# Kernel tuning notes

Measured on AMD Instinct MI355X. Metric: run time of the kernel, lower is better.

## Reference

```python
import jax, jax.numpy as jnp
import numpy as np
from jax import lax

N_TRACES = 128
TRACE_LEN = 32          # uniform trace length -> seq_len
INPUT_DIM = 64
HIDDEN_DIM = 128
BATCH = N_TRACES * TRACE_LEN  # 4096 events = batch_size


def setup_inputs() -> dict:
    key = jax.random.key(0)
    ks = jax.random.split(key, 12)
    s = 1.0 / np.sqrt(HIDDEN_DIM)
    u = lambda k, shape: jax.random.uniform(k, shape, jnp.float32, -s, s)
    return {
        "input": jax.random.normal(ks[0], (BATCH, INPUT_DIM), jnp.float32),
        # layer 0 LSTM params (gate order i,f,g,o as in torch)
        "W_ih0": u(ks[1], (4 * HIDDEN_DIM, INPUT_DIM)),
        "W_hh0": u(ks[2], (4 * HIDDEN_DIM, HIDDEN_DIM)),
        "b_ih0": u(ks[3], (4 * HIDDEN_DIM,)),
        "b_hh0": u(ks[4], (4 * HIDDEN_DIM,)),
        # layer 1 LSTM params
        "W_ih1": u(ks[5], (4 * HIDDEN_DIM, HIDDEN_DIM)),
        "W_hh1": u(ks[6], (4 * HIDDEN_DIM, HIDDEN_DIM)),
        "b_ih1": u(ks[7], (4 * HIDDEN_DIM,)),
        "b_hh1": u(ks[8], (4 * HIDDEN_DIM,)),
        # final linear: hidden -> 1
        "W_lin": u(ks[9], (1, HIDDEN_DIM)),
        "b_lin": u(ks[10], (1,)),
    }


def _lstm_layer(xs, W_ih, W_hh, b_ih, b_hh):
    # xs: [T, B, D_in] time-major. Returns hidden stream [T, B, H].
    H = W_hh.shape[1]
    B = xs.shape[1]
    # precompute input projection for all timesteps
    x_proj = jnp.einsum('tbd,gd->tbg', xs, W_ih) + b_ih + b_hh  # [T,B,4H]

    def step(carry, xp):
        h, c = carry
        gates = xp + h @ W_hh.T                # [B,4H]
        i, f, g, o = jnp.split(gates, 4, axis=-1)
        i = jax.nn.sigmoid(i)
        f = jax.nn.sigmoid(f)
        g = jnp.tanh(g)
        o = jax.nn.sigmoid(o)
        c = f * c + i * g
        h = o * jnp.tanh(c)
        return (h, c), h

    h0 = jnp.zeros((B, H), xs.dtype)
    _, hs = lax.scan(step, (h0, h0), x_proj)
    return hs


def _forward(input, W_ih0, W_hh0, b_ih0, b_hh0, W_ih1, W_hh1, b_ih1, b_hh1, W_lin, b_lin):
    L, D = TRACE_LEN, INPUT_DIM
    # Prefix scatter: event k of a trace gets the padded prefix events[0..k].
    x_tr = input.reshape(N_TRACES, L, D)                       # [Ntr, L, D]
    causal = (jnp.arange(L)[None, :] <= jnp.arange(L)[:, None])  # [k, j] mask j<=k
    padded = x_tr[:, None, :, :] * causal[None, :, :, None].astype(input.dtype)  # [Ntr,L(k),L(j),D]
    padded = padded.reshape(BATCH, L, D)                       # batch-first padded sequences

    xs = jnp.transpose(padded, (1, 0, 2))                      # [L, B, D] time-major
    h1 = _lstm_layer(xs, W_ih0, W_hh0, b_ih0, b_hh0)           # [L, B, H]
    h2 = _lstm_layer(h1, W_ih1, W_hh1, b_ih1, b_hh1)           # [L, B, H]

    out = jnp.einsum('tbh,oh->tbo', h2, W_lin) + b_lin         # [L, B, 1]
    # last valid timestep gather: lengths[i]-1 = (i mod L)
    lens_m1 = jnp.tile(jnp.arange(L), N_TRACES)                # [B]
    y_pred = out[lens_m1, jnp.arange(BATCH), 0]                # [B]
    return y_pred


def reference(input, W_ih0, W_hh0, b_ih0, b_hh0, W_ih1, W_hh1, b_ih1, b_hh1, W_lin, b_lin):
    return _forward(input, W_ih0, W_hh0, b_ih0, b_hh0, W_ih1, W_hh1, b_ih1, b_hh1, W_lin, b_lin)
```

## Files before the change

kernel.cpp:

```cpp
#include <hip/hip_runtime.h>

#define N_TRACES 128
#define TLEN 32
#define IN_DIM 64
#define HID 128
#define G4 (4 * HID)
#define BATCH (N_TRACES * TLEN)
#define HROW 160


__device__ __forceinline__ float fast_sigmoid(float x) {
    return 1.0f / (1.0f + __expf(-x));
}
__device__ __forceinline__ float fast_tanh(float x) {
    return 1.0f - 2.0f / (__expf(2.0f * x) + 1.0f);
}
__device__ __forceinline__ float oct_reduce(float x) {
    x += __int_as_float(__builtin_amdgcn_update_dpp(
        0, __float_as_int(x), 0xB1 , 0xF, 0xF, true));
    x += __int_as_float(__builtin_amdgcn_update_dpp(
        0, __float_as_int(x), 0x4E , 0xF, 0xF, true));
    x += __int_as_float(__builtin_amdgcn_update_dpp(
        0, __float_as_int(x), 0x141 , 0xF, 0xF, true));
    return x;
}

__device__ __forceinline__ void load_w16(const float* __restrict__ W, int u, int s,
                                         float (&w)[4][16]) {
    #pragma unroll
    for (int i = 0; i < 4; ++i) {
        const float* wr = W + (size_t)(u + 128 * i) * HID + 16 * s;
        #pragma unroll
        for (int j = 0; j < 4; ++j) {
            float4 v = *(const float4*)(wr + 4 * j);
            w[i][4 * j + 0] = v.x; w[i][4 * j + 1] = v.y;
            w[i][4 * j + 2] = v.z; w[i][4 * j + 3] = v.w;
        }
    }
    #pragma unroll
    for (int i = 0; i < 4; ++i)
        #pragma unroll
        for (int j = 0; j < 16; ++j)
            asm volatile("" : "+v"(w[i][j]));
}

__device__ __forceinline__ void matvec_acc16(const float (&w)[4][16],
                                             const float* hb, float (&acc)[4]) {
    #pragma unroll
    for (int j = 0; j < 4; ++j) {
        float4 v = *(const float4*)(hb + 4 * j);
        float hx[4] = {v.x, v.y, v.z, v.w};
        #pragma unroll
        for (int e = 0; e < 4; ++e) {
            #pragma unroll
            for (int i = 0; i < 4; ++i)
                acc[i] = fmaf(w[i][4 * j + e], hx[e], acc[i]);
        }
    }
}


template <int K>
__global__ __launch_bounds__(256) void gemm_bt(
    const float* __restrict__ A,
    const float* __restrict__ W,
    const float* __restrict__ b1,
    const float* __restrict__ b2,
    float* __restrict__ out,
    int Nld)
{
    constexpr int LD = 68;
    __shared__ float At[K][LD];
    __shared__ float Wt[K][LD];

    const int tid = threadIdx.x;
    const int m0 = blockIdx.x * 64;
    const int n0 = blockIdx.y * 64;

    const int rot = tid & 3;
    #pragma unroll
    for (int j = 0; j < K / 16; ++j) {
        const int e = 4 * (tid + 256 * j);
        const int row = e / K;
        const int k = e % K;
        float4 va = *(const float4*)(A + (size_t)(m0 + row) * K + k);
        float4 vw = *(const float4*)(W + (size_t)(n0 + row) * K + k);
        float fa[4] = {va.x, va.y, va.z, va.w};
        float fw[4] = {vw.x, vw.y, vw.z, vw.w};
        #pragma unroll
        for (int ii = 0; ii < 4; ++ii) {
            const int i = (ii + rot) & 3;
            At[k + i][row] = fa[i];
            Wt[k + i][row] = fw[i];
        }
    }
    __syncthreads();

    const int tx = tid & 15;
    const int ty = tid >> 4;
    float acc[4][4] = {};

    #pragma unroll 4
    for (int k = 0; k < K; ++k) {
        float4 a = *(const float4*)&At[k][ty * 4];
        float4 w = *(const float4*)&Wt[k][tx * 4];
        acc[0][0] = fmaf(a.x, w.x, acc[0][0]); acc[0][1] = fmaf(a.x, w.y, acc[0][1]);
        acc[0][2] = fmaf(a.x, w.z, acc[0][2]); acc[0][3] = fmaf(a.x, w.w, acc[0][3]);
        acc[1][0] = fmaf(a.y, w.x, acc[1][0]); acc[1][1] = fmaf(a.y, w.y, acc[1][1]);
        acc[1][2] = fmaf(a.y, w.z, acc[1][2]); acc[1][3] = fmaf(a.y, w.w, acc[1][3]);
        acc[2][0] = fmaf(a.z, w.x, acc[2][0]); acc[2][1] = fmaf(a.z, w.y, acc[2][1]);
        acc[2][2] = fmaf(a.z, w.z, acc[2][2]); acc[2][3] = fmaf(a.z, w.w, acc[2][3]);
        acc[3][0] = fmaf(a.w, w.x, acc[3][0]); acc[3][1] = fmaf(a.w, w.y, acc[3][1]);
        acc[3][2] = fmaf(a.w, w.z, acc[3][2]); acc[3][3] = fmaf(a.w, w.w, acc[3][3]);
    }

    float bb[4];
    #pragma unroll
    for (int j = 0; j < 4; ++j) {
        const int n = n0 + tx * 4 + j;
        bb[j] = b1[n] + b2[n];
    }
    #pragma unroll
    for (int i = 0; i < 4; ++i) {
        const int m = m0 + ty * 4 + i;
        float4 v;
        v.x = acc[i][0] + bb[0]; v.y = acc[i][1] + bb[1];
        v.z = acc[i][2] + bb[2]; v.w = acc[i][3] + bb[3];
        *(float4*)(out + (size_t)m * Nld + n0 + tx * 4) = v;
    }
}


__global__ __launch_bounds__(1024) void fused_trace(
    const float* __restrict__ xproj0,
    const float* __restrict__ Whh0,
    const float* __restrict__ Wih1,
    const float* __restrict__ bih1,
    const float* __restrict__ bhh1,
    const float* __restrict__ Whh1,
    const float* __restrict__ Wlin,
    const float* __restrict__ blin,
    float* __restrict__ y)
{
    const int trace = blockIdx.x;
    const int tid = threadIdx.x;
    const int u = tid >> 3;
    const int s = tid & 7;
    const int hw = 20 * (u >> 4) + (u & 15);

    __shared__ __align__(16) float hs[TLEN][HROW];
    __shared__ __align__(16) float xp[TLEN * G4];

    float w[4][16];

    const float* xpb = xproj0 + (size_t)trace * TLEN * G4;
    #pragma unroll
    for (int j = 0; j < 4; ++j) {
        const int f4 = j * 1024 + tid;
        *(float4*)(&xp[4 * f4]) = *(const float4*)(xpb + 4 * f4);
    }
    load_w16(Whh0, u, s, w);
    __syncthreads();

    float c = 0.0f;
    #pragma unroll 1
    for (int t = 0; t < TLEN; ++t) {
        float xg[4];
        #pragma unroll
        for (int i = 0; i < 4; ++i) xg[i] = xp[t * G4 + 128 * i + u];

        float acc[4] = {0.f, 0.f, 0.f, 0.f};
        if (t > 0) matvec_acc16(w, &hs[t - 1][20 * s], acc);
        #pragma unroll
        for (int i = 0; i < 4; ++i) acc[i] = oct_reduce(acc[i]);

        const float iv = fast_sigmoid(acc[0] + xg[0]);
        const float fv = fast_sigmoid(acc[1] + xg[1]);
        const float gv = fast_tanh(acc[2] + xg[2]);
        const float ov = fast_sigmoid(acc[3] + xg[3]);
        c = fv * c + iv * gv;
        const float h = ov * fast_tanh(c);
        if (s == 0) hs[t][hw] = h;
        __syncthreads();
    }

    load_w16(Wih1, u, s, w);
    float bi[4];
    #pragma unroll
    for (int i = 0; i < 4; ++i) bi[i] = bih1[u + 128 * i] + bhh1[u + 128 * i];
    #pragma unroll 1
    for (int t = 0; t < TLEN; ++t) {
        float acc[4] = {0.f, 0.f, 0.f, 0.f};
        matvec_acc16(w, &hs[t][20 * s], acc);
        #pragma unroll
        for (int i = 0; i < 4; ++i) acc[i] = oct_reduce(acc[i]);
        if (s == 0) {
            #pragma unroll
            for (int i = 0; i < 4; ++i) xp[t * G4 + 128 * i + u] = acc[i] + bi[i];
        }
    }
    __syncthreads();

    load_w16(Whh1, u, s, w);
    c = 0.0f;
    #pragma unroll 1
    for (int t = 0; t < TLEN; ++t) {
        float xg[4];
        #pragma unroll
        for (int i = 0; i < 4; ++i) xg[i] = xp[t * G4 + 128 * i + u];

        float acc[4] = {0.f, 0.f, 0.f, 0.f};
        if (t > 0) matvec_acc16(w, &hs[t - 1][20 * s], acc);
        #pragma unroll
        for (int i = 0; i < 4; ++i) acc[i] = oct_reduce(acc[i]);

        const float iv = fast_sigmoid(acc[0] + xg[0]);
        const float fv = fast_sigmoid(acc[1] + xg[1]);
        const float gv = fast_tanh(acc[2] + xg[2]);
        const float ov = fast_sigmoid(acc[3] + xg[3]);
        c = fv * c + iv * gv;
        const float h = ov * fast_tanh(c);
        if (s == 0) hs[t][hw] = h;
        __syncthreads();
    }

    if (tid < 256) {
        const int tq = tid >> 3;
        const int sq = tid & 7;
        float wl[16];
        #pragma unroll
        for (int j = 0; j < 4; ++j) {
            float4 v = *(const float4*)(Wlin + 16 * sq + 4 * j);
            wl[4 * j + 0] = v.x; wl[4 * j + 1] = v.y;
            wl[4 * j + 2] = v.z; wl[4 * j + 3] = v.w;
        }
        const float* hb = &hs[tq][20 * sq];
        float a = 0.f;
        #pragma unroll
        for (int j = 0; j < 4; ++j) {
            float4 v = *(const float4*)(hb + 4 * j);
            a = fmaf(v.x, wl[4 * j + 0], a);
            a = fmaf(v.y, wl[4 * j + 1], a);
            a = fmaf(v.z, wl[4 * j + 2], a);
            a = fmaf(v.w, wl[4 * j + 3], a);
        }
        a = oct_reduce(a);
        if (sq == 0) y[trace * TLEN + tq] = a + blin[0];
    }
}


extern "C" void kernel_launch(void* const* d_in, const int* in_sizes, int n_in,
                              void* d_out, int out_size, void* d_ws, size_t ws_size,
                              hipStream_t stream) {
    const float* input = (const float*)d_in[0];
    const float* W_ih0 = (const float*)d_in[1];
    const float* W_hh0 = (const float*)d_in[2];
    const float* b_ih0 = (const float*)d_in[3];
    const float* b_hh0 = (const float*)d_in[4];
    const float* W_ih1 = (const float*)d_in[5];
    const float* W_hh1 = (const float*)d_in[6];
    const float* b_ih1 = (const float*)d_in[7];
    const float* b_hh1 = (const float*)d_in[8];
    const float* W_lin = (const float*)d_in[9];
    const float* b_lin = (const float*)d_in[10];
    float* out = (float*)d_out;

    float* xproj0 = (float*)d_ws;

    dim3 ggrid(BATCH / 64, G4 / 64);

    gemm_bt<IN_DIM><<<ggrid, 256, 0, stream>>>(input, W_ih0, b_ih0, b_hh0, xproj0, G4);
    fused_trace<<<N_TRACES, 1024, 0, stream>>>(xproj0, W_hh0, W_ih1, b_ih1, b_hh1,
                                               W_hh1, W_lin, b_lin, out);
}
```

Before: 180.5 us.

## Compute two hidden units per thread and halve fused LSTM block size

Each thread in the fused per-trace LSTM kernel now owns two adjacent hidden units instead of one, and the block shrinks from 1024 to 512 threads. Each h vector read from LDS is reused for twice as many FMAs, and the eight independent accumulators give more instruction-level parallelism. Fewer waves should also make each per-timestep barrier cheaper. The input-gate values for the next step are prefetched from LDS before the barrier, and h and xp are stored as float2. The cost is doubled register use for weights (128 floats per thread) and twice the serial work per thread on each step.

```diff
diff --git a/kernel.cpp b/kernel.cpp
--- a/kernel.cpp
+++ b/kernel.cpp
@@ -25,36 +25,43 @@
     return x;
 }
 
-__device__ __forceinline__ void load_w16(const float* __restrict__ W, int u, int s,
-                                         float (&w)[4][16]) {
-    #pragma unroll
-    for (int i = 0; i < 4; ++i) {
-        const float* wr = W + (size_t)(u + 128 * i) * HID + 16 * s;
-        #pragma unroll
-        for (int j = 0; j < 4; ++j) {
-            float4 v = *(const float4*)(wr + 4 * j);
-            w[i][4 * j + 0] = v.x; w[i][4 * j + 1] = v.y;
-            w[i][4 * j + 2] = v.z; w[i][4 * j + 3] = v.w;
-        }
-    }
-    #pragma unroll
-    for (int i = 0; i < 4; ++i)
-        #pragma unroll
-        for (int j = 0; j < 16; ++j)
-            asm volatile("" : "+v"(w[i][j]));
-}
-
-__device__ __forceinline__ void matvec_acc16(const float (&w)[4][16],
-                                             const float* hb, float (&acc)[4]) {
-    #pragma unroll
-    for (int j = 0; j < 4; ++j) {
-        float4 v = *(const float4*)(hb + 4 * j);
+__device__ __forceinline__ void load_w8(const float* __restrict__ W, int u0, int s,
+                                        float (&w)[2][4][16]) {
+    #pragma unroll
+    for (int j = 0; j < 2; ++j) {
+        #pragma unroll
+        for (int i = 0; i < 4; ++i) {
+            const float* wr = W + (size_t)(u0 + j + 128 * i) * HID + 16 * s;
+            #pragma unroll
+            for (int q = 0; q < 4; ++q) {
+                float4 v = *(const float4*)(wr + 4 * q);
+                w[j][i][4 * q + 0] = v.x; w[j][i][4 * q + 1] = v.y;
+                w[j][i][4 * q + 2] = v.z; w[j][i][4 * q + 3] = v.w;
+            }
+        }
+    }
+    #pragma unroll
+    for (int j = 0; j < 2; ++j)
+        #pragma unroll
+        for (int i = 0; i < 4; ++i)
+            #pragma unroll
+            for (int k = 0; k < 16; ++k)
+                asm volatile("" : "+v"(w[j][i][k]));
+}
+
+__device__ __forceinline__ void matvec8(const float (&w)[2][4][16],
+                                        const float* hb, float (&acc)[2][4]) {
+    #pragma unroll
+    for (int q = 0; q < 4; ++q) {
+        float4 v = *(const float4*)(hb + 4 * q);
         float hx[4] = {v.x, v.y, v.z, v.w};
         #pragma unroll
         for (int e = 0; e < 4; ++e) {
             #pragma unroll
-            for (int i = 0; i < 4; ++i)
-                acc[i] = fmaf(w[i][4 * j + e], hx[e], acc[i]);
+            for (int j = 0; j < 2; ++j)
+                #pragma unroll
+                for (int i = 0; i < 4; ++i)
+                    acc[j][i] = fmaf(w[j][i][4 * q + e], hx[e], acc[j][i]);
         }
     }
 }
@@ -131,7 +138,7 @@
 }
 
 
-__global__ __launch_bounds__(1024) void fused_trace(
+__global__ __launch_bounds__(512) void fused_trace(
     const float* __restrict__ xproj0,
     const float* __restrict__ Whh0,
     const float* __restrict__ Wih1,
@@ -144,83 +151,124 @@
 {
     const int trace = blockIdx.x;
     const int tid = threadIdx.x;
-    const int u = tid >> 3;
+    const int ub = tid >> 3;
     const int s = tid & 7;
-    const int hw = 20 * (u >> 4) + (u & 15);
+    const int u0 = 2 * ub;
+    const int hw = 20 * (u0 >> 4) + (u0 & 15);
 
     __shared__ __align__(16) float hs[TLEN][HROW];
     __shared__ __align__(16) float xp[TLEN * G4];
 
-    float w[4][16];
+    float w[2][4][16];
 
     const float* xpb = xproj0 + (size_t)trace * TLEN * G4;
     #pragma unroll
-    for (int j = 0; j < 4; ++j) {
-        const int f4 = j * 1024 + tid;
+    for (int j = 0; j < 8; ++j) {
+        const int f4 = j * 512 + tid;
         *(float4*)(&xp[4 * f4]) = *(const float4*)(xpb + 4 * f4);
     }
-    load_w16(Whh0, u, s, w);
+    load_w8(Whh0, u0, s, w);
     __syncthreads();
 
-    float c = 0.0f;
+    float2 xgn[4];
+    #pragma unroll
+    for (int i = 0; i < 4; ++i) xgn[i] = *(const float2*)&xp[128 * i + u0];
+    float c0 = 0.0f, c1 = 0.0f;
     #pragma unroll 1
     for (int t = 0; t < TLEN; ++t) {
-        float xg[4];
-        #pragma unroll
-        for (int i = 0; i < 4; ++i) xg[i] = xp[t * G4 + 128 * i + u];
-
-        float acc[4] = {0.f, 0.f, 0.f, 0.f};
-        if (t > 0) matvec_acc16(w, &hs[t - 1][20 * s], acc);
-        #pragma unroll
-        for (int i = 0; i < 4; ++i) acc[i] = oct_reduce(acc[i]);
-
-        const float iv = fast_sigmoid(acc[0] + xg[0]);
-        const float fv = fast_sigmoid(acc[1] + xg[1]);
-        const float gv = fast_tanh(acc[2] + xg[2]);
-        const float ov = fast_sigmoid(acc[3] + xg[3]);
-        c = fv * c + iv * gv;
-        const float h = ov * fast_tanh(c);
-        if (s == 0) hs[t][hw] = h;
+        float2 xg[4];
+        #pragma unroll
+        for (int i = 0; i < 4; ++i) xg[i] = xgn[i];
+
+        float acc[2][4] = {};
+        if (t > 0) matvec8(w, &hs[t - 1][20 * s], acc);
+        #pragma unroll
+        for (int j = 0; j < 2; ++j)
+            #pragma unroll
+            for (int i = 0; i < 4; ++i) acc[j][i] = oct_reduce(acc[j][i]);
+
+        const float i0 = fast_sigmoid(acc[0][0] + xg[0].x);
+        const float f0 = fast_sigmoid(acc[0][1] + xg[1].x);
+        const float g0 = fast_tanh   (acc[0][2] + xg[2].x);
+        const float o0 = fast_sigmoid(acc[0][3] + xg[3].x);
+        c0 = f0 * c0 + i0 * g0;
+        const float h0 = o0 * fast_tanh(c0);
+        const float i1 = fast_sigmoid(acc[1][0] + xg[0].y);
+        const float f1 = fast_sigmoid(acc[1][1] + xg[1].y);
+        const float g1 = fast_tanh   (acc[1][2] + xg[2].y);
+        const float o1 = fast_sigmoid(acc[1][3] + xg[3].y);
+        c1 = f1 * c1 + i1 * g1;
+        const float h1 = o1 * fast_tanh(c1);
+        if (s == 0) *(float2*)&hs[t][hw] = make_float2(h0, h1);
+
+        if (t < TLEN - 1) {
+            #pragma unroll
+            for (int i = 0; i < 4; ++i)
+                xgn[i] = *(const float2*)&xp[(t + 1) * G4 + 128 * i + u0];
+        }
         __syncthreads();
     }
 
-    load_w16(Wih1, u, s, w);
-    float bi[4];
-    #pragma unroll
-    for (int i = 0; i < 4; ++i) bi[i] = bih1[u + 128 * i] + bhh1[u + 128 * i];
+    load_w8(Wih1, u0, s, w);
+    float bi[2][4];
+    #pragma unroll
+    for (int j = 0; j < 2; ++j)
+        #pragma unroll
+        for (int i = 0; i < 4; ++i)
+            bi[j][i] = bih1[u0 + j + 128 * i] + bhh1[u0 + j + 128 * i];
     #pragma unroll 1
     for (int t = 0; t < TLEN; ++t) {
-        float acc[4] = {0.f, 0.f, 0.f, 0.f};
-        matvec_acc16(w, &hs[t][20 * s], acc);
-        #pragma unroll
-        for (int i = 0; i < 4; ++i) acc[i] = oct_reduce(acc[i]);
+        float acc[2][4] = {};
+        matvec8(w, &hs[t][20 * s], acc);
+        #pragma unroll
+        for (int j = 0; j < 2; ++j)
+            #pragma unroll
+            for (int i = 0; i < 4; ++i) acc[j][i] = oct_reduce(acc[j][i]);
         if (s == 0) {
             #pragma unroll
-            for (int i = 0; i < 4; ++i) xp[t * G4 + 128 * i + u] = acc[i] + bi[i];
+            for (int i = 0; i < 4; ++i)
+                *(float2*)&xp[t * G4 + 128 * i + u0] =
+                    make_float2(acc[0][i] + bi[0][i], acc[1][i] + bi[1][i]);
         }
     }
     __syncthreads();
 
-    load_w16(Whh1, u, s, w);
-    c = 0.0f;
+    load_w8(Whh1, u0, s, w);
+    #pragma unroll
+    for (int i = 0; i < 4; ++i) xgn[i] = *(const float2*)&xp[128 * i + u0];
+    c0 = 0.0f; c1 = 0.0f;
     #pragma unroll 1
     for (int t = 0; t < TLEN; ++t) {
-        float xg[4];
-        #pragma unroll
-        for (int i = 0; i < 4; ++i) xg[i] = xp[t * G4 + 128 * i + u];
-
-        float acc[4] = {0.f, 0.f, 0.f, 0.f};
-        if (t > 0) matvec_acc16(w, &hs[t - 1][20 * s], acc);
-        #pragma unroll
-        for (int i = 0; i < 4; ++i) acc[i] = oct_reduce(acc[i]);
-
-        const float iv = fast_sigmoid(acc[0] + xg[0]);
-        const float fv = fast_sigmoid(acc[1] + xg[1]);
-        const float gv = fast_tanh(acc[2] + xg[2]);
-        const float ov = fast_sigmoid(acc[3] + xg[3]);
-        c = fv * c + iv * gv;
-        const float h = ov * fast_tanh(c);
-        if (s == 0) hs[t][hw] = h;
+        float2 xg[4];
+        #pragma unroll
+        for (int i = 0; i < 4; ++i) xg[i] = xgn[i];
+
+        float acc[2][4] = {};
+        if (t > 0) matvec8(w, &hs[t - 1][20 * s], acc);
+        #pragma unroll
+        for (int j = 0; j < 2; ++j)
+            #pragma unroll
+            for (int i = 0; i < 4; ++i) acc[j][i] = oct_reduce(acc[j][i]);
+
+        const float i0 = fast_sigmoid(acc[0][0] + xg[0].x);
+        const float f0 = fast_sigmoid(acc[0][1] + xg[1].x);
+        const float g0 = fast_tanh   (acc[0][2] + xg[2].x);
+        const float o0 = fast_sigmoid(acc[0][3] + xg[3].x);
+        c0 = f0 * c0 + i0 * g0;
+        const float h0 = o0 * fast_tanh(c0);
+        const float i1 = fast_sigmoid(acc[1][0] + xg[0].y);
+        const float f1 = fast_sigmoid(acc[1][1] + xg[1].y);
+        const float g1 = fast_tanh   (acc[1][2] + xg[2].y);
+        const float o1 = fast_sigmoid(acc[1][3] + xg[3].y);
+        c1 = f1 * c1 + i1 * g1;
+        const float h1 = o1 * fast_tanh(c1);
+        if (s == 0) *(float2*)&hs[t][hw] = make_float2(h0, h1);
+
+        if (t < TLEN - 1) {
+            #pragma unroll
+            for (int i = 0; i < 4; ++i)
+                xgn[i] = *(const float2*)&xp[(t + 1) * G4 + 128 * i + u0];
+        }
         __syncthreads();
     }
 
@@ -271,6 +319,6 @@
     dim3 ggrid(BATCH / 64, G4 / 64);
 
     gemm_bt<IN_DIM><<<ggrid, 256, 0, stream>>>(input, W_ih0, b_ih0, b_hh0, xproj0, G4);
-    fused_trace<<<N_TRACES, 1024, 0, stream>>>(xproj0, W_hh0, W_ih1, b_ih1, b_hh1,
-                                               W_hh1, W_lin, b_lin, out);
-}
+    fused_trace<<<N_TRACES, 512, 0, stream>>>(xproj0, W_hh0, W_ih1, b_ih1, b_hh1,
+                                              W_hh1, W_lin, b_lin, out);
+}
```

Measured after the change: 182.2 us. No clear change (+1.0%).
